# Optimization experiments

Measured on AMD Instinct MI355X. Metric: run time of the kernel, lower is better.

## Reference

```python
import jax, jax.numpy as jnp
import numpy as np

N = 4_194_304  # number of sample points


def _make_C():
    # Faithful reproduction of the module's compliance matrix (including the
    # asymmetry: Ci[2,0]=Ci[2,1]=-vp, NOT -vp/Ep, exactly as in the source).
    vp, Ep = 0.4, 0.21
    Ci = np.zeros((6, 6), dtype=np.float64)
    Ci[0, 0] = 1 / Ep;  Ci[0, 1] = -vp / Ep; Ci[0, 2] = -vp / Ep
    Ci[1, 0] = -vp / Ep; Ci[1, 1] = 1 / Ep;  Ci[1, 2] = -vp / Ep
    Ci[2, 0] = -vp;      Ci[2, 1] = -vp;     Ci[2, 2] = 1 / Ep
    Ci[3, 3] = 2 * (1 + vp) / Ep
    Ci[4, 4] = 2 * (1 + vp) / Ep
    Ci[5, 5] = 2 * (1 + vp) / Ep
    return jnp.asarray(np.linalg.inv(Ci), dtype=jnp.float32)

_C = _make_C()  # [6, 6] stiffness matrix


def setup_inputs() -> dict:
    key = jax.random.key(0)
    k1, k2, k3, k4 = jax.random.split(key, 4)
    return {
        "grad_u": jax.random.normal(k1, (N, 3), dtype=jnp.float32),
        "grad_v": jax.random.normal(k2, (N, 3), dtype=jnp.float32),
        "grad_w": jax.random.normal(k3, (N, 3), dtype=jnp.float32),
        "gt_sdf": jax.random.normal(k4, (N,), dtype=jnp.float32),
    }


def reference(grad_u, grad_v, grad_w, gt_sdf):
    # Build per-point strain tensor in Voigt-like notation: [N, 6]
    et = jnp.stack([
        grad_u[:, 0],
        grad_v[:, 1],
        grad_w[:, 2],
        (grad_u[:, 1] + grad_v[:, 0]) * 0.5,
        (grad_u[:, 2] + grad_w[:, 0]) * 0.5,
        (grad_w[:, 1] + grad_v[:, 2]) * 0.5,
    ], axis=1)
    # Per-point quadratic form et_i^T C et_i == diag(et @ C @ et.T) without the
    # O(N^2) intermediate the torch code materializes.
    q = jnp.einsum('ni,ij,nj->n', et, _C, et)
    # Mask = points with gt_sdf < 1e-8 (index_select in torch; masked here so
    # shapes stay static under jit). Excluded points contribute 0 to the norm.
    mask = gt_sdf < 1e-8
    qm = jnp.where(mask, q, 0.0)
    count = jnp.sum(mask).astype(et.dtype)  # et.shape[0] after index_select
    W = jnp.sqrt(jnp.sum(qm * qm))           # L2 norm of the diagonal vector
    return W / count
```

## Files before the change

kernel.cpp:

```cpp
#include <hip/hip_runtime.h>
#include <math.h>

struct CParams {
    float b[3][3];
    float s;
};

static CParams make_C() {
    const double vp = 0.4, Ep = 0.21;
    double A[3][3] = {
        {1.0 / Ep, -vp / Ep, -vp / Ep},
        {-vp / Ep, 1.0 / Ep, -vp / Ep},
        {-vp,      -vp,      1.0 / Ep},
    };
    double inv[3][3] = {{1, 0, 0}, {0, 1, 0}, {0, 0, 1}};
    for (int col = 0; col < 3; ++col) {
        int piv = col;
        for (int r = col + 1; r < 3; ++r)
            if (fabs(A[r][col]) > fabs(A[piv][col])) piv = r;
        if (piv != col) {
            for (int c = 0; c < 3; ++c) {
                double t = A[col][c]; A[col][c] = A[piv][c]; A[piv][c] = t;
                t = inv[col][c]; inv[col][c] = inv[piv][c]; inv[piv][c] = t;
            }
        }
        double d = A[col][col];
        for (int c = 0; c < 3; ++c) { A[col][c] /= d; inv[col][c] /= d; }
        for (int r = 0; r < 3; ++r) {
            if (r == col) continue;
            double f = A[r][col];
            for (int c = 0; c < 3; ++c) {
                A[r][c] -= f * A[col][c];
                inv[r][c] -= f * inv[col][c];
            }
        }
    }
    CParams p;
    for (int i = 0; i < 3; ++i)
        for (int j = 0; j < 3; ++j)
            p.b[i][j] = (float)inv[i][j];
    p.s = (float)(Ep / (2.0 * (1.0 + vp)));
    return p;
}

static const CParams g_C = make_C();

#define MAXB 2048
#define TPB  256

typedef float vfloat4 __attribute__((ext_vector_type(4)));

__device__ __forceinline__ float4 ntload4(const float* p) {
    vfloat4 v = __builtin_nontemporal_load((const vfloat4*)p);
    return make_float4(v.x, v.y, v.z, v.w);
}

__device__ __forceinline__ void accum_point(
    float u0, float u1, float u2,
    float v0, float v1, float v2,
    float w0, float w1, float w2,
    float sd, const CParams& C, float& sumq2, float& cnt)
{
    float e0 = u0, e1 = v1, e2 = w2;
    float e3 = 0.5f * (u1 + v0);
    float e4 = 0.5f * (u2 + w0);
    float e5 = 0.5f * (w1 + v2);

    float q = e0 * (C.b[0][0] * e0 + C.b[0][1] * e1 + C.b[0][2] * e2)
            + e1 * (C.b[1][0] * e0 + C.b[1][1] * e1 + C.b[1][2] * e2)
            + e2 * (C.b[2][0] * e0 + C.b[2][1] * e1 + C.b[2][2] * e2)
            + C.s * (e3 * e3 + e4 * e4 + e5 * e5);

    bool m = sd < 1e-8f;
    float qm = m ? q : 0.0f;
    sumq2 += qm * qm;
    cnt   += m ? 1.0f : 0.0f;
}

__global__ __launch_bounds__(TPB) void biomech_reduce(
    const float* __restrict__ gu, const float* __restrict__ gv,
    const float* __restrict__ gw, const float* __restrict__ gs,
    float* __restrict__ ws, int n, CParams C)
{
    const int tid    = blockIdx.x * TPB + threadIdx.x;
    const int stride = gridDim.x * TPB;
    const int nvec   = n >> 2;

    float sumq2 = 0.0f, cnt = 0.0f;

    for (int i = tid; i < nvec; i += stride) {
        const float* pu = gu + 12 * i;
        const float* pv = gv + 12 * i;
        const float* pw = gw + 12 * i;
        float4 a0 = ntload4(pu), a1 = ntload4(pu + 4), a2 = ntload4(pu + 8);
        float4 b0 = ntload4(pv), b1 = ntload4(pv + 4), b2 = ntload4(pv + 8);
        float4 c0 = ntload4(pw), c1 = ntload4(pw + 4), c2 = ntload4(pw + 8);
        float4 sd = ntload4(gs + 4 * i);

        accum_point(a0.x, a0.y, a0.z,  b0.x, b0.y, b0.z,  c0.x, c0.y, c0.z,
                    sd.x, C, sumq2, cnt);
        accum_point(a0.w, a1.x, a1.y,  b0.w, b1.x, b1.y,  c0.w, c1.x, c1.y,
                    sd.y, C, sumq2, cnt);
        accum_point(a1.z, a1.w, a2.x,  b1.z, b1.w, b2.x,  c1.z, c1.w, c2.x,
                    sd.z, C, sumq2, cnt);
        accum_point(a2.y, a2.z, a2.w,  b2.y, b2.z, b2.w,  c2.y, c2.z, c2.w,
                    sd.w, C, sumq2, cnt);
    }

    if (blockIdx.x == 0 && threadIdx.x == 0) {
        for (int i = nvec * 4; i < n; ++i) {
            accum_point(gu[3 * i], gu[3 * i + 1], gu[3 * i + 2],
                        gv[3 * i], gv[3 * i + 1], gv[3 * i + 2],
                        gw[3 * i], gw[3 * i + 1], gw[3 * i + 2],
                        gs[i], C, sumq2, cnt);
        }
    }

#pragma unroll
    for (int off = 32; off > 0; off >>= 1) {
        sumq2 += __shfl_down(sumq2, off);
        cnt   += __shfl_down(cnt, off);
    }

    __shared__ float ssum[TPB / 64], scnt[TPB / 64];
    const int wave = threadIdx.x >> 6;
    const int lane = threadIdx.x & 63;
    if (lane == 0) { ssum[wave] = sumq2; scnt[wave] = cnt; }
    __syncthreads();
    if (threadIdx.x == 0) {
        float s2 = 0.0f, c2 = 0.0f;
#pragma unroll
        for (int i = 0; i < TPB / 64; ++i) { s2 += ssum[i]; c2 += scnt[i]; }
        ws[blockIdx.x]        = s2;
        ws[MAXB + blockIdx.x] = c2;
    }
}

__global__ __launch_bounds__(256) void biomech_finalize(
    const float* __restrict__ ws, float* __restrict__ out, int nb)
{
    float s = 0.0f, c = 0.0f;
    for (int i = threadIdx.x; i < nb; i += 256) {
        s += ws[i];
        c += ws[MAXB + i];
    }
#pragma unroll
    for (int off = 32; off > 0; off >>= 1) {
        s += __shfl_down(s, off);
        c += __shfl_down(c, off);
    }
    __shared__ float ssum[4], scnt[4];
    const int wave = threadIdx.x >> 6;
    const int lane = threadIdx.x & 63;
    if (lane == 0) { ssum[wave] = s; scnt[wave] = c; }
    __syncthreads();
    if (threadIdx.x == 0) {
        float s2 = ssum[0] + ssum[1] + ssum[2] + ssum[3];
        float c2 = scnt[0] + scnt[1] + scnt[2] + scnt[3];
        out[0] = sqrtf(s2) / c2;
    }
}

extern "C" void kernel_launch(void* const* d_in, const int* in_sizes, int n_in,
                              void* d_out, int out_size, void* d_ws, size_t ws_size,
                              hipStream_t stream) {
    const float* gu = (const float*)d_in[0];
    const float* gv = (const float*)d_in[1];
    const float* gw = (const float*)d_in[2];
    const float* gs = (const float*)d_in[3];
    float* ws = (float*)d_ws;
    float* out = (float*)d_out;

    const int n = in_sizes[3];
    const int nvec = n >> 2;

    int grid = (nvec + TPB - 1) / TPB;
    if (grid > 2048) grid = 2048;
    if (grid > MAXB) grid = MAXB;
    while (grid > 1 && (size_t)(MAXB + grid) * sizeof(float) > ws_size) grid >>= 1;
    if (grid < 1) grid = 1;

    biomech_reduce<<<grid, TPB, 0, stream>>>(gu, gv, gw, gs, ws, n, g_C);
    biomech_finalize<<<1, 256, 0, stream>>>(ws, out, grid);
}
```

Before: 177.1 us.

## Stage AoS gradient loads through per-wave LDS for coalesced float4 reads

```diff
diff --git a/kernel.cpp b/kernel.cpp
--- a/kernel.cpp
+++ b/kernel.cpp
@@ -45,8 +45,14 @@
 
 static const CParams g_C = make_C();
 
-#define MAXB 2048
-#define TPB  256
+#define MAXB  2048
+#define TPB   256
+#define WPB   (TPB / 64)
+#define CHUNK 256
+#define TILEP (WPB * CHUNK)
+#define F4PW  192
+
+#define WAVE_FENCE() asm volatile("" ::: "memory")
 
 typedef float vfloat4 __attribute__((ext_vector_type(4)));
 
@@ -82,33 +88,57 @@
     const float* __restrict__ gw, const float* __restrict__ gs,
     float* __restrict__ ws, int n, CParams C)
 {
-    const int tid    = blockIdx.x * TPB + threadIdx.x;
-    const int stride = gridDim.x * TPB;
-    const int nvec   = n >> 2;
+    __shared__ float4 buf[WPB][3][F4PW];
+
+    const int wave = threadIdx.x >> 6;
+    const int lane = threadIdx.x & 63;
+    const int ntiles = n / TILEP;
+
+    float4* lu = &buf[wave][0][0];
+    float4* lv = &buf[wave][1][0];
+    float4* lw = &buf[wave][2][0];
 
     float sumq2 = 0.0f, cnt = 0.0f;
 
-    for (int i = tid; i < nvec; i += stride) {
-        const float* pu = gu + 12 * i;
-        const float* pv = gv + 12 * i;
-        const float* pw = gw + 12 * i;
-        float4 a0 = ntload4(pu), a1 = ntload4(pu + 4), a2 = ntload4(pu + 8);
-        float4 b0 = ntload4(pv), b1 = ntload4(pv + 4), b2 = ntload4(pv + 8);
-        float4 c0 = ntload4(pw), c1 = ntload4(pw + 4), c2 = ntload4(pw + 8);
-        float4 sd = ntload4(gs + 4 * i);
+    for (int t = blockIdx.x; t < ntiles; t += gridDim.x) {
+        const int gb = t * (TILEP * 3 / 4) + wave * F4PW;
+        const int sb = t * (TILEP / 4)     + wave * 64;
+
+        float4 A0 = ntload4(gu + 4 * (gb + lane));
+        float4 A1 = ntload4(gu + 4 * (gb + 64 + lane));
+        float4 A2 = ntload4(gu + 4 * (gb + 128 + lane));
+        float4 B0 = ntload4(gv + 4 * (gb + lane));
+        float4 B1 = ntload4(gv + 4 * (gb + 64 + lane));
+        float4 B2 = ntload4(gv + 4 * (gb + 128 + lane));
+        float4 C0 = ntload4(gw + 4 * (gb + lane));
+        float4 C1 = ntload4(gw + 4 * (gb + 64 + lane));
+        float4 C2 = ntload4(gw + 4 * (gb + 128 + lane));
+        float4 SD = ntload4(gs + 4 * (sb + lane));
+
+        lu[lane] = A0; lu[64 + lane] = A1; lu[128 + lane] = A2;
+        lv[lane] = B0; lv[64 + lane] = B1; lv[128 + lane] = B2;
+        lw[lane] = C0; lw[64 + lane] = C1; lw[128 + lane] = C2;
+
+        WAVE_FENCE();
+
+        float4 a0 = lu[3 * lane], a1 = lu[3 * lane + 1], a2 = lu[3 * lane + 2];
+        float4 b0 = lv[3 * lane], b1 = lv[3 * lane + 1], b2 = lv[3 * lane + 2];
+        float4 c0 = lw[3 * lane], c1 = lw[3 * lane + 1], c2 = lw[3 * lane + 2];
+
+        WAVE_FENCE();
 
         accum_point(a0.x, a0.y, a0.z,  b0.x, b0.y, b0.z,  c0.x, c0.y, c0.z,
-                    sd.x, C, sumq2, cnt);
+                    SD.x, C, sumq2, cnt);
         accum_point(a0.w, a1.x, a1.y,  b0.w, b1.x, b1.y,  c0.w, c1.x, c1.y,
-                    sd.y, C, sumq2, cnt);
+                    SD.y, C, sumq2, cnt);
         accum_point(a1.z, a1.w, a2.x,  b1.z, b1.w, b2.x,  c1.z, c1.w, c2.x,
-                    sd.z, C, sumq2, cnt);
+                    SD.z, C, sumq2, cnt);
         accum_point(a2.y, a2.z, a2.w,  b2.y, b2.z, b2.w,  c2.y, c2.z, c2.w,
-                    sd.w, C, sumq2, cnt);
+                    SD.w, C, sumq2, cnt);
     }
 
     if (blockIdx.x == 0 && threadIdx.x == 0) {
-        for (int i = nvec * 4; i < n; ++i) {
+        for (int i = ntiles * TILEP; i < n; ++i) {
             accum_point(gu[3 * i], gu[3 * i + 1], gu[3 * i + 2],
                         gv[3 * i], gv[3 * i + 1], gv[3 * i + 2],
                         gw[3 * i], gw[3 * i + 1], gw[3 * i + 2],
@@ -122,15 +152,13 @@
         cnt   += __shfl_down(cnt, off);
     }
 
-    __shared__ float ssum[TPB / 64], scnt[TPB / 64];
-    const int wave = threadIdx.x >> 6;
-    const int lane = threadIdx.x & 63;
+    __shared__ float ssum[WPB], scnt[WPB];
     if (lane == 0) { ssum[wave] = sumq2; scnt[wave] = cnt; }
     __syncthreads();
     if (threadIdx.x == 0) {
         float s2 = 0.0f, c2 = 0.0f;
 #pragma unroll
-        for (int i = 0; i < TPB / 64; ++i) { s2 += ssum[i]; c2 += scnt[i]; }
+        for (int i = 0; i < WPB; ++i) { s2 += ssum[i]; c2 += scnt[i]; }
         ws[blockIdx.x]        = s2;
         ws[MAXB + blockIdx.x] = c2;
     }
@@ -172,9 +200,9 @@
     float* out = (float*)d_out;
 
     const int n = in_sizes[3];
-    const int nvec = n >> 2;
-
-    int grid = (nvec + TPB - 1) / TPB;
+    const int ntiles = n / TILEP;
+
+    int grid = ntiles > 0 ? ntiles : 1;
     if (grid > 2048) grid = 2048;
     if (grid > MAXB) grid = MAXB;
     while (grid > 1 && (size_t)(MAXB + grid) * sizeof(float) > ws_size) grid >>= 1;
```

Result: faster. 160.9 us (-9.1%).
